# Kernel optimization log

Hardware: AMD Instinct MI355X
Metric: run time of the kernel (lower is better)

Reference implementation:

```python
import jax, jax.numpy as jnp
import numpy as np

B, L, KD, ED, H = 8, 4096, 512, 1024, 8  # batch, seq, key_dim, embed_dim, n_heads
LN_EPS = 1e-5


def setup_inputs() -> dict:
    key = jax.random.key(0)
    ks = jax.random.split(key, 6)
    keys = jax.random.normal(ks[0], (B, L, KD), dtype=jnp.float32)
    values = jax.random.normal(ks[1], (B, L, ED), dtype=jnp.float32)
    # learned params
    query = jax.random.normal(ks[2], (H, 1, KD // H), dtype=jnp.float32) * 0.02
    k_bias = jax.random.normal(ks[3], (KD,), dtype=jnp.float32) / np.sqrt(KD).astype(np.float32)
    v_bias = jnp.zeros((ED,), dtype=jnp.float32)
    softmax_weight = 1.0 + 0.01 * jax.random.normal(ks[4], (H, 1, L + 1), dtype=jnp.float32)
    softmax_bias = 0.01 * jax.random.normal(ks[5], (H, 1, L + 1), dtype=jnp.float32)
    gamma = jnp.ones((ED,), dtype=jnp.float32)
    beta = jnp.zeros((ED,), dtype=jnp.float32)
    return {"keys": keys, "values": values, "query": query, "k_bias": k_bias,
            "v_bias": v_bias, "softmax_weight": softmax_weight,
            "softmax_bias": softmax_bias, "gamma": gamma, "beta": beta}


def reference(keys, values, query, k_bias, v_bias, softmax_weight, softmax_bias, gamma, beta):
    b = keys.shape[0]
    # append learned bias token to keys and values  -> [B, L+1, *]
    keys = jnp.concatenate([keys, jnp.broadcast_to(k_bias, (b, 1, k_bias.shape[0]))], axis=1)
    values = jnp.concatenate([values, jnp.broadcast_to(v_bias, (b, 1, v_bias.shape[0]))], axis=1)
    lp = keys.shape[1]
    # torch multihead_reshape is a raw contiguous view [B,L,C] -> [B*H, L, C/H]
    K = keys.reshape(b * H, lp, keys.shape[2] // H)      # [B*H, L+1, KD/H]
    V = values.reshape(b * H, lp, values.shape[2] // H)  # [B*H, L+1, ED/H]
    Q = jnp.tile(query, (b, 1, 1))                       # [B*H, 1, KD/H]
    scores = jnp.einsum('bqd,bld->bql', Q, K)            # [B*H, 1, L+1]
    scores = scores * jnp.tile(softmax_weight, (b, 1, 1)) + jnp.tile(softmax_bias, (b, 1, 1))
    attn = jax.nn.softmax(scores, axis=-1)               # [B*H, 1, L+1]
    A = jnp.einsum('bql,bld->bqd', attn, V)              # [B*H, 1, ED/H]
    A = A.reshape(b, 1, -1)                              # multihead_unshape -> [B, 1, ED]
    # LayerNorm over embed dim (torch default eps=1e-5, biased var)
    mean = jnp.mean(A, axis=-1, keepdims=True)
    var = jnp.var(A, axis=-1, keepdims=True)
    return (A - mean) * jax.lax.rsqrt(var + LN_EPS) * gamma + beta
```

## Files before the change

kernel.cpp:

```cpp
#include <hip/hip_runtime.h>

#define BATCH 8
#define LSEQ  4096
#define LP    4097
#define KDIM  512
#define EDIM  1024
#define NH    8
#define DK    64
#define DV    128
#define NG    64
#define NC    32
#define LN_EPS 1e-5f

typedef float floatx4 __attribute__((ext_vector_type(4)));

__global__ __launch_bounds__(256) void lqa_fused_kernel(
    const float* __restrict__ keys, const float* __restrict__ k_bias,
    const float* __restrict__ values, const float* __restrict__ v_bias,
    const float* __restrict__ query, const float* __restrict__ sw,
    const float* __restrict__ sb, float* __restrict__ partials,
    float* __restrict__ zstats)
{
    const int cg = blockIdx.x;
    const int g  = blockIdx.y;
    const int b = g >> 3, h = g & 7;
    const int t = threadIdx.x;
    const int w = t >> 6;
    const int lane = t & 63;
    const int row0 = cg * 128 + w * 32;

    __shared__ float red[4 * DV];
    __shared__ float zred[4];

    const int gid = lane >> 4, l16 = lane & 15;
    const floatx4 q = *reinterpret_cast<const floatx4*>(query + h * DK + l16 * 4);
    const float* kp = keys + (long long)b * (LSEQ * KDIM);
    const int fheadk = h * (LP * DK);
    const float* wptr = sw + h * LP;
    const float* bptr = sb + h * LP;
    float e[8];
    float z = 0.f;
#pragma unroll
    for (int j = 0; j < 8; ++j) {
        const int row = row0 + 4 * j + gid;
        const int f = fheadk + row * DK;
        const float* rowp = (f < LSEQ * KDIM) ? (kp + f)
                                              : (k_bias + (f - LSEQ * KDIM));
        const floatx4 k = *reinterpret_cast<const floatx4*>(rowp + l16 * 4);
        float s = q.x * k.x + q.y * k.y + q.z * k.z + q.w * k.w;
        s += __shfl_xor(s, 1);
        s += __shfl_xor(s, 2);
        s += __shfl_xor(s, 4);
        s += __shfl_xor(s, 8);
        const float ev = __expf(s * wptr[row] + bptr[row]);
        e[j] = ev;
        z += ev;
    }
    z += __shfl_xor(z, 16);
    z += __shfl_xor(z, 32);

    const int hi = (lane >> 5) & 1;
    const int d0 = (lane & 31) * 4;
    const float* vp = values + (long long)b * (LSEQ * EDIM);
    const int fheadv = h * (LP * DV);
    float a0 = 0.f, a1 = 0.f, a2 = 0.f, a3 = 0.f;
#pragma unroll
    for (int j = 0; j < 8; ++j) {
        const float e0 = __shfl(e[j], 16 * hi, 64);
        const float e1 = __shfl(e[j], 16 * (2 + hi), 64);
        {
            const int row = row0 + 4 * j + hi;
            const int f = fheadv + row * DV;
            const float* rowp = (f < LSEQ * EDIM) ? (vp + f)
                                                  : (v_bias + (f - LSEQ * EDIM));
            const floatx4 v = *reinterpret_cast<const floatx4*>(rowp + d0);
            a0 += e0 * v.x; a1 += e0 * v.y; a2 += e0 * v.z; a3 += e0 * v.w;
        }
        {
            const int row = row0 + 4 * j + 2 + hi;
            const int f = fheadv + row * DV;
            const float* rowp = (f < LSEQ * EDIM) ? (vp + f)
                                                  : (v_bias + (f - LSEQ * EDIM));
            const floatx4 v = *reinterpret_cast<const floatx4*>(rowp + d0);
            a0 += e1 * v.x; a1 += e1 * v.y; a2 += e1 * v.z; a3 += e1 * v.w;
        }
    }
    a0 += __shfl_xor(a0, 32);
    a1 += __shfl_xor(a1, 32);
    a2 += __shfl_xor(a2, 32);
    a3 += __shfl_xor(a3, 32);

    if (lane < 32) {
        float* dst = red + w * DV + d0;
        dst[0] = a0; dst[1] = a1; dst[2] = a2; dst[3] = a3;
    }
    if (lane == 0) zred[w] = z;
    __syncthreads();
    if (t < DV) {
        const float sum = red[t] + red[DV + t] + red[2 * DV + t] + red[3 * DV + t];
        partials[((long long)(g * NC + cg)) * DV + t] = sum;
    } else if (t == DV) {
        zstats[g * NC + cg] = zred[0] + zred[1] + zred[2] + zred[3];
    }
}

__global__ __launch_bounds__(1024) void lqa_combine_ln_kernel(
    const float* __restrict__ partials, const float* __restrict__ zstats,
    const float* __restrict__ keys, const float* __restrict__ values,
    const float* __restrict__ k_bias, const float* __restrict__ v_bias,
    const float* __restrict__ query, const float* __restrict__ sw,
    const float* __restrict__ sb, const float* __restrict__ gamma,
    const float* __restrict__ beta, float* __restrict__ out)
{
    const int b = blockIdx.x;
    const int t = threadIdx.x;
    __shared__ float zh[NH];
    __shared__ float eb[NH];
    __shared__ float r1[16], r2[16];

    if (t < 256) {
        float zv = zstats[(b * NH + (t >> 5)) * NC + (t & 31)];
        zv += __shfl_xor(zv, 1);
        zv += __shfl_xor(zv, 2);
        zv += __shfl_xor(zv, 4);
        zv += __shfl_xor(zv, 8);
        zv += __shfl_xor(zv, 16);
        if ((t & 31) == 0) zh[t >> 5] = zv;
    } else if (t < 384) {
        const int tt = t - 256;
        const int h = tt >> 4, l16 = tt & 15;
        const floatx4 q = *reinterpret_cast<const floatx4*>(query + h * DK + l16 * 4);
        const int fk = h * (LP * DK) + LSEQ * DK;
        const float* kr = (fk < LSEQ * KDIM)
            ? keys + (long long)b * (LSEQ * KDIM) + fk
            : k_bias + (fk - LSEQ * KDIM);
        const floatx4 k = *reinterpret_cast<const floatx4*>(kr + l16 * 4);
        float s = q.x * k.x + q.y * k.y + q.z * k.z + q.w * k.w;
        s += __shfl_xor(s, 1);
        s += __shfl_xor(s, 2);
        s += __shfl_xor(s, 4);
        s += __shfl_xor(s, 8);
        if (l16 == 0) eb[h] = __expf(s * sw[h * LP + LSEQ] + sb[h * LP + LSEQ]);
    }
    __syncthreads();
    if (t < NH) zh[t] += eb[t];
    __syncthreads();

    const int h = t >> 7, d = t & 127;
    const float* src = partials + ((long long)((b * NH + h) * NC)) * DV + d;
    float sum = 0.f;
#pragma unroll
    for (int c = 0; c < NC; ++c) sum += src[c * DV];
    const int fv = h * (LP * DV) + LSEQ * DV + d;
    const float v4 = (fv < LSEQ * EDIM)
        ? values[(long long)b * (LSEQ * EDIM) + fv]
        : v_bias[fv - LSEQ * EDIM];
    const float av = (sum + eb[h] * v4) / zh[h];

    float s1 = av, s2 = av * av;
    s1 += __shfl_xor(s1, 1);  s2 += __shfl_xor(s2, 1);
    s1 += __shfl_xor(s1, 2);  s2 += __shfl_xor(s2, 2);
    s1 += __shfl_xor(s1, 4);  s2 += __shfl_xor(s2, 4);
    s1 += __shfl_xor(s1, 8);  s2 += __shfl_xor(s2, 8);
    s1 += __shfl_xor(s1, 16); s2 += __shfl_xor(s2, 16);
    s1 += __shfl_xor(s1, 32); s2 += __shfl_xor(s2, 32);
    if ((t & 63) == 0) { r1[t >> 6] = s1; r2[t >> 6] = s2; }
    __syncthreads();
    float fs1 = 0.f, fs2 = 0.f;
#pragma unroll
    for (int i = 0; i < 16; ++i) { fs1 += r1[i]; fs2 += r2[i]; }
    const float mean = fs1 * (1.0f / EDIM);
    const float var = fs2 * (1.0f / EDIM) - mean * mean;
    const float inv = rsqrtf(var + LN_EPS);
    out[(long long)b * EDIM + t] = (av - mean) * inv * gamma[t] + beta[t];
}

extern "C" void kernel_launch(void* const* d_in, const int* in_sizes, int n_in,
                              void* d_out, int out_size, void* d_ws, size_t ws_size,
                              hipStream_t stream) {
    const float* keys   = (const float*)d_in[0];
    const float* values = (const float*)d_in[1];
    const float* query  = (const float*)d_in[2];
    const float* k_bias = (const float*)d_in[3];
    const float* v_bias = (const float*)d_in[4];
    const float* sw     = (const float*)d_in[5];
    const float* sb     = (const float*)d_in[6];
    const float* gamma  = (const float*)d_in[7];
    const float* beta   = (const float*)d_in[8];
    float* out = (float*)d_out;

    float* ws = (float*)d_ws;
    float* partials = ws;
    float* zstats = ws + (long long)NG * NC * DV;

    lqa_fused_kernel<<<dim3(NC, NG), 256, 0, stream>>>(
        keys, k_bias, values, v_bias, query, sw, sb, partials, zstats);
    lqa_combine_ln_kernel<<<BATCH, 1024, 0, stream>>>(
        partials, zstats, keys, values, k_bias, v_bias, query, sw, sb,
        gamma, beta, out);
}
```

Before: 253.2 us.

## Software-pipeline K/V loads with double-buffered registers and halve chunk count

The attention kernel now handles 64 rows per wave instead of 32, in stages of 8 rows. Two register buffers alternate so the key/value loads for the next stage are issued before the current stage's scores, exp and value accumulation, with sched_barriers to keep that order. The grid shrinks from 32 to 16 chunks per head, which halves the partials the combine kernel reads. The aim is more memory-level parallelism and less latency exposure in a bandwidth-bound stream, at the cost of more registers and fewer blocks.

```diff
diff --git a/kernel.cpp b/kernel.cpp
--- a/kernel.cpp
+++ b/kernel.cpp
@@ -9,12 +9,59 @@
 #define DK    64
 #define DV    128
 #define NG    64
-#define NC    32
+#define NCH   16
+#define KLIM  (LSEQ * KDIM)
+#define VLIM  (LSEQ * EDIM)
 #define LN_EPS 1e-5f
 
 typedef float floatx4 __attribute__((ext_vector_type(4)));
 
-__global__ __launch_bounds__(256) void lqa_fused_kernel(
+#define STAGE_LOAD(S, rr) do {                                              \
+    const int rk0 = (rr) + gid;                                             \
+    const int rk1 = (rr) + 4 + gid;                                         \
+    const int f0 = fheadk + rk0 * DK;                                       \
+    const int f1 = fheadk + rk1 * DK;                                       \
+    const float* p0 = (f0 < KLIM) ? (kp + f0) : (k_bias + (f0 - KLIM));     \
+    const float* p1 = (f1 < KLIM) ? (kp + f1) : (k_bias + (f1 - KLIM));     \
+    kv0##S = *reinterpret_cast<const floatx4*>(p0 + l16 * 4);               \
+    kv1##S = *reinterpret_cast<const floatx4*>(p1 + l16 * 4);               \
+    wv0##S = wptr[rk0]; bv0##S = bptr[rk0];                                 \
+    wv1##S = wptr[rk1]; bv1##S = bptr[rk1];                                 \
+    _Pragma("unroll")                                                       \
+    for (int j = 0; j < 4; ++j) {                                           \
+        const int fv = fheadv + ((rr) + 2 * j + hi) * DV;                   \
+        const float* pv = (fv < VLIM) ? (vp + fv) : (v_bias + (fv - VLIM)); \
+        vv##S[j] = *reinterpret_cast<const floatx4*>(pv + d0);              \
+    }                                                                       \
+} while (0)
+
+#define STAGE_COMPUTE(S) do {                                               \
+    float s0 = q.x * kv0##S.x + q.y * kv0##S.y + q.z * kv0##S.z + q.w * kv0##S.w; \
+    float s1 = q.x * kv1##S.x + q.y * kv1##S.y + q.z * kv1##S.z + q.w * kv1##S.w; \
+    s0 += __shfl_xor(s0, 1); s1 += __shfl_xor(s1, 1);                       \
+    s0 += __shfl_xor(s0, 2); s1 += __shfl_xor(s1, 2);                       \
+    s0 += __shfl_xor(s0, 4); s1 += __shfl_xor(s1, 4);                       \
+    s0 += __shfl_xor(s0, 8); s1 += __shfl_xor(s1, 8);                       \
+    const float e0 = __expf(s0 * wv0##S + bv0##S);                          \
+    const float e1 = __expf(s1 * wv1##S + bv1##S);                          \
+    z += e0 + e1;                                                           \
+    const float w0 = __shfl(e0, 16 * hi, 64);                               \
+    const float w1 = __shfl(e0, 16 * (2 + hi), 64);                         \
+    const float w2 = __shfl(e1, 16 * hi, 64);                               \
+    const float w3 = __shfl(e1, 16 * (2 + hi), 64);                         \
+    a0 += w0 * vv##S[0].x; a1 += w0 * vv##S[0].y;                           \
+    a2 += w0 * vv##S[0].z; a3 += w0 * vv##S[0].w;                           \
+    a0 += w1 * vv##S[1].x; a1 += w1 * vv##S[1].y;                           \
+    a2 += w1 * vv##S[1].z; a3 += w1 * vv##S[1].w;                           \
+    a0 += w2 * vv##S[2].x; a1 += w2 * vv##S[2].y;                           \
+    a2 += w2 * vv##S[2].z; a3 += w2 * vv##S[2].w;                           \
+    a0 += w3 * vv##S[3].x; a1 += w3 * vv##S[3].y;                           \
+    a2 += w3 * vv##S[3].z; a3 += w3 * vv##S[3].w;                           \
+} while (0)
+
+#define SB __builtin_amdgcn_sched_barrier(0)
+
+__global__ __launch_bounds__(256, 4) void lqa_fused_kernel(
     const float* __restrict__ keys, const float* __restrict__ k_bias,
     const float* __restrict__ values, const float* __restrict__ v_bias,
     const float* __restrict__ query, const float* __restrict__ sw,
@@ -27,68 +74,48 @@
     const int t = threadIdx.x;
     const int w = t >> 6;
     const int lane = t & 63;
-    const int row0 = cg * 128 + w * 32;
+    const int R0 = cg * 256 + w * 64;
 
     __shared__ float red[4 * DV];
     __shared__ float zred[4];
 
     const int gid = lane >> 4, l16 = lane & 15;
-    const floatx4 q = *reinterpret_cast<const floatx4*>(query + h * DK + l16 * 4);
+    const int hi = (lane >> 5) & 1;
+    const int d0 = (lane & 31) * 4;
+
     const float* kp = keys + (long long)b * (LSEQ * KDIM);
+    const float* vp = values + (long long)b * (LSEQ * EDIM);
     const int fheadk = h * (LP * DK);
+    const int fheadv = h * (LP * DV);
     const float* wptr = sw + h * LP;
     const float* bptr = sb + h * LP;
-    float e[8];
-    float z = 0.f;
-#pragma unroll
-    for (int j = 0; j < 8; ++j) {
-        const int row = row0 + 4 * j + gid;
-        const int f = fheadk + row * DK;
-        const float* rowp = (f < LSEQ * KDIM) ? (kp + f)
-                                              : (k_bias + (f - LSEQ * KDIM));
-        const floatx4 k = *reinterpret_cast<const floatx4*>(rowp + l16 * 4);
-        float s = q.x * k.x + q.y * k.y + q.z * k.z + q.w * k.w;
-        s += __shfl_xor(s, 1);
-        s += __shfl_xor(s, 2);
-        s += __shfl_xor(s, 4);
-        s += __shfl_xor(s, 8);
-        const float ev = __expf(s * wptr[row] + bptr[row]);
-        e[j] = ev;
-        z += ev;
-    }
-    z += __shfl_xor(z, 16);
-    z += __shfl_xor(z, 32);
-
-    const int hi = (lane >> 5) & 1;
-    const int d0 = (lane & 31) * 4;
-    const float* vp = values + (long long)b * (LSEQ * EDIM);
-    const int fheadv = h * (LP * DV);
-    float a0 = 0.f, a1 = 0.f, a2 = 0.f, a3 = 0.f;
-#pragma unroll
-    for (int j = 0; j < 8; ++j) {
-        const float e0 = __shfl(e[j], 16 * hi, 64);
-        const float e1 = __shfl(e[j], 16 * (2 + hi), 64);
-        {
-            const int row = row0 + 4 * j + hi;
-            const int f = fheadv + row * DV;
-            const float* rowp = (f < LSEQ * EDIM) ? (vp + f)
-                                                  : (v_bias + (f - LSEQ * EDIM));
-            const floatx4 v = *reinterpret_cast<const floatx4*>(rowp + d0);
-            a0 += e0 * v.x; a1 += e0 * v.y; a2 += e0 * v.z; a3 += e0 * v.w;
-        }
-        {
-            const int row = row0 + 4 * j + 2 + hi;
-            const int f = fheadv + row * DV;
-            const float* rowp = (f < LSEQ * EDIM) ? (vp + f)
-                                                  : (v_bias + (f - LSEQ * EDIM));
-            const floatx4 v = *reinterpret_cast<const floatx4*>(rowp + d0);
-            a0 += e1 * v.x; a1 += e1 * v.y; a2 += e1 * v.z; a3 += e1 * v.w;
-        }
-    }
+    const floatx4 q = *reinterpret_cast<const floatx4*>(query + h * DK + l16 * 4);
+
+    floatx4 kv0A, kv1A, vvA[4];
+    floatx4 kv0B, kv1B, vvB[4];
+    float wv0A, wv1A, bv0A, bv1A;
+    float wv0B, wv1B, bv0B, bv1B;
+    float a0 = 0.f, a1 = 0.f, a2 = 0.f, a3 = 0.f, z = 0.f;
+
+    STAGE_LOAD(A, R0 + 0);
+    STAGE_LOAD(B, R0 + 8);
+    SB;
+    STAGE_COMPUTE(A);
+    STAGE_LOAD(A, R0 + 16); SB; STAGE_COMPUTE(B);
+    STAGE_LOAD(B, R0 + 24); SB; STAGE_COMPUTE(A);
+    STAGE_LOAD(A, R0 + 32); SB; STAGE_COMPUTE(B);
+    STAGE_LOAD(B, R0 + 40); SB; STAGE_COMPUTE(A);
+    STAGE_LOAD(A, R0 + 48); SB; STAGE_COMPUTE(B);
+    STAGE_LOAD(B, R0 + 56); SB; STAGE_COMPUTE(A);
+    SB;
+    STAGE_COMPUTE(B);
+
     a0 += __shfl_xor(a0, 32);
     a1 += __shfl_xor(a1, 32);
     a2 += __shfl_xor(a2, 32);
     a3 += __shfl_xor(a3, 32);
+    z += __shfl_xor(z, 16);
+    z += __shfl_xor(z, 32);
 
     if (lane < 32) {
         float* dst = red + w * DV + d0;
@@ -98,9 +125,9 @@
     __syncthreads();
     if (t < DV) {
         const float sum = red[t] + red[DV + t] + red[2 * DV + t] + red[3 * DV + t];
-        partials[((long long)(g * NC + cg)) * DV + t] = sum;
+        partials[((long long)(g * NCH + cg)) * DV + t] = sum;
     } else if (t == DV) {
-        zstats[g * NC + cg] = zred[0] + zred[1] + zred[2] + zred[3];
+        zstats[g * NCH + cg] = zred[0] + zred[1] + zred[2] + zred[3];
     }
 }
 
@@ -118,22 +145,21 @@
     __shared__ float eb[NH];
     __shared__ float r1[16], r2[16];
 
-    if (t < 256) {
-        float zv = zstats[(b * NH + (t >> 5)) * NC + (t & 31)];
+    if (t < 128) {
+        float zv = zstats[(b * NH + (t >> 4)) * NCH + (t & 15)];
         zv += __shfl_xor(zv, 1);
         zv += __shfl_xor(zv, 2);
         zv += __shfl_xor(zv, 4);
         zv += __shfl_xor(zv, 8);
-        zv += __shfl_xor(zv, 16);
-        if ((t & 31) == 0) zh[t >> 5] = zv;
-    } else if (t < 384) {
-        const int tt = t - 256;
+        if ((t & 15) == 0) zh[t >> 4] = zv;
+    } else if (t < 256) {
+        const int tt = t - 128;
         const int h = tt >> 4, l16 = tt & 15;
         const floatx4 q = *reinterpret_cast<const floatx4*>(query + h * DK + l16 * 4);
         const int fk = h * (LP * DK) + LSEQ * DK;
-        const float* kr = (fk < LSEQ * KDIM)
+        const float* kr = (fk < KLIM)
             ? keys + (long long)b * (LSEQ * KDIM) + fk
-            : k_bias + (fk - LSEQ * KDIM);
+            : k_bias + (fk - KLIM);
         const floatx4 k = *reinterpret_cast<const floatx4*>(kr + l16 * 4);
         float s = q.x * k.x + q.y * k.y + q.z * k.z + q.w * k.w;
         s += __shfl_xor(s, 1);
@@ -147,14 +173,14 @@
     __syncthreads();
 
     const int h = t >> 7, d = t & 127;
-    const float* src = partials + ((long long)((b * NH + h) * NC)) * DV + d;
+    const float* src = partials + ((long long)((b * NH + h) * NCH)) * DV + d;
     float sum = 0.f;
 #pragma unroll
-    for (int c = 0; c < NC; ++c) sum += src[c * DV];
+    for (int c = 0; c < NCH; ++c) sum += src[c * DV];
     const int fv = h * (LP * DV) + LSEQ * DV + d;
-    const float v4 = (fv < LSEQ * EDIM)
+    const float v4 = (fv < VLIM)
         ? values[(long long)b * (LSEQ * EDIM) + fv]
-        : v_bias[fv - LSEQ * EDIM];
+        : v_bias[fv - VLIM];
     const float av = (sum + eb[h] * v4) / zh[h];
 
     float s1 = av, s2 = av * av;
@@ -191,9 +217,9 @@
 
     float* ws = (float*)d_ws;
     float* partials = ws;
-    float* zstats = ws + (long long)NG * NC * DV;
-
-    lqa_fused_kernel<<<dim3(NC, NG), 256, 0, stream>>>(
+    float* zstats = ws + (long long)NG * NCH * DV;
+
+    lqa_fused_kernel<<<dim3(NCH, NG), 256, 0, stream>>>(
         keys, k_bias, values, v_bias, query, sw, sb, partials, zstats);
     lqa_combine_ln_kernel<<<BATCH, 1024, 0, stream>>>(
         partials, zstats, keys, values, k_bias, v_bias, query, sw, sb,
```

After: 275.9 us. 1.09x slower.
